# Performance work log

Hardware: AMD Instinct MI355X
Metric: run time of the kernel (lower is better)

## Reference

```python
import jax, jax.numpy as jnp
import numpy as np

B, IN_E, IN_I, D = 4096, 4096, 4096, 2048
IN_BR = 8192
BS = IN_BR // D  # block size = 4
K_E, K_I = 50, 1
E_TO_I = 50.0
BN_EPS = 1e-5


def setup_inputs() -> dict:
    key = jax.random.key(0)
    ks = jax.random.split(key, 8)
    # fan-in uniform init like nn.Linear (kaiming-uniform bound ~ 1/sqrt(in))
    def linw(k, out_f, in_f):
        b = 1.0 / np.sqrt(in_f)
        return jax.random.uniform(k, (out_f, in_f), jnp.float32, -b, b)
    return {
        "excitatory_input": jax.random.normal(ks[0], (B, IN_E), jnp.float32),
        "inhibitory_input": jax.random.normal(ks[1], (B, IN_I), jnp.float32),
        "dendrite_branch_outputs": jax.random.uniform(ks[2], (B, IN_BR), jnp.float32),
        "w_exc": linw(ks[3], D, IN_E),
        "w_inh": linw(ks[4], D, IN_I),
        "w_block": linw(ks[5], D, IN_BR),
        "bn_gamma": jnp.ones((D,), jnp.float32),
        "bn_beta": jnp.zeros((D,), jnp.float32),
    }


def _topk_linear(x, w, k):
    # keep the k largest weights per output row, zero the rest, then matmul
    idx = jax.lax.top_k(w, k)[1]                          # [D, k]
    mask = jnp.zeros_like(w).at[jnp.arange(w.shape[0])[:, None], idx].set(1.0)
    return x @ (w * mask).T                               # [B, D]


def _block_linear(x, w):
    # block-diagonal mask: row c uses columns [c*BS, (c+1)*BS)
    out_f = w.shape[0]
    wb = w.reshape(out_f, out_f, BS)[jnp.arange(out_f), jnp.arange(out_f)]  # [D, BS]
    xb = x.reshape(x.shape[0], out_f, BS)                                   # [B, D, BS]
    return jnp.einsum('bds,ds->bd', xb, wb)


def reference(excitatory_input, inhibitory_input, dendrite_branch_outputs,
              w_exc, w_inh, w_block, bn_gamma, bn_beta):
    dendrite_excitation = _topk_linear(excitatory_input, w_exc, K_E)
    dendrite_inhibition = _topk_linear(inhibitory_input, w_inh, K_I)
    dendrite_depolarization = _block_linear(dendrite_branch_outputs, w_block)
    total_excitatory = dendrite_excitation + dendrite_depolarization
    # neuron_type == 'excitatory'
    act = total_excitatory - E_TO_I * dendrite_inhibition
    # BatchNorm1d, training mode: batch stats, biased variance
    mean = jnp.mean(act, axis=0)
    var = jnp.var(act, axis=0)
    act = (act - mean) * jax.lax.rsqrt(var + BN_EPS) * bn_gamma + bn_beta
    return jax.nn.sigmoid(act)
```

## Files before the change

kernel.cpp:

```cpp
#include <hip/hip_runtime.h>
#include <hip/hip_fp16.h>

#define B_     4096
#define INE_   4096
#define INBR_  8192
#define D_     2048
#define KE_    50
#define KPAD_  52
#define CAP_   512

__device__ __forceinline__ unsigned packh2(float a, float b) {
  __half2 h = __floats2half2_rn(a, b);
  return __builtin_bit_cast(unsigned, h);
}
__device__ __forceinline__ float2 unpackh2(unsigned u) {
  __half2 h = __builtin_bit_cast(__half2, u);
  return __half22float2(h);
}

__global__ __launch_bounds__(256) void extract_diag(
    const float* __restrict__ wblock, float* __restrict__ wdiag)
{
  int d = blockIdx.x * 256 + threadIdx.x;
  float4 w = *reinterpret_cast<const float4*>(wblock + (size_t)d * (INBR_ + 4));
  reinterpret_cast<float4*>(wdiag)[d] = w;
}

__global__ __launch_bounds__(256) void topk_kernel(
    const float* __restrict__ W, int k, int kpad, float hi, float t0,
    float vscale, unsigned* __restrict__ out_off, float* __restrict__ out_val)
{
  const int row = blockIdx.x;
  const int t   = threadIdx.x;
  const float* wr = W + (size_t)row * INE_;

  __shared__ float cval[CAP_];
  __shared__ int   ccol[CAP_];
  __shared__ int   scnt;
  __shared__ int   red[4];

  float thr = t0;
  int M = 0;
  for (int attempt = 0; attempt < 8; ++attempt) {
    int local = 0;
    #pragma unroll
    for (int j = 0; j < 4; ++j) {
      float4 w4 = *reinterpret_cast<const float4*>(wr + 4 * (t + 256 * j));
      local += (w4.x > thr) + (w4.y > thr) + (w4.z > thr) + (w4.w > thr);
    }
    #pragma unroll
    for (int off = 32; off > 0; off >>= 1) local += __shfl_down(local, off);
    if ((t & 63) == 0) red[t >> 6] = local;
    __syncthreads();
    M = red[0] + red[1] + red[2] + red[3];
    __syncthreads();
    if (M >= k && M <= CAP_) break;
    if (M < k) thr = hi - (hi - thr) * 4.0f;
    else       thr = hi - (hi - thr) * 0.5f;
  }

  if (t == 0) scnt = 0;
  __syncthreads();
  #pragma unroll
  for (int j = 0; j < 4; ++j) {
    int cbase = 4 * (t + 256 * j);
    float4 w4 = *reinterpret_cast<const float4*>(wr + cbase);
    float wv[4] = {w4.x, w4.y, w4.z, w4.w};
    #pragma unroll
    for (int q = 0; q < 4; ++q) {
      if (wv[q] > thr) {
        int p = atomicAdd(&scnt, 1);
        if (p < CAP_) { cval[p] = wv[q]; ccol[p] = cbase + q; }
      }
    }
  }
  __syncthreads();
  M = scnt < CAP_ ? scnt : CAP_;

  for (int i = t; i < M; i += 256) {
    float wi = cval[i]; int ci = ccol[i];
    int rank = 0;
    for (int m = 0; m < M; ++m) {
      float wm = cval[m]; int cm = ccol[m];
      rank += (wm > wi || (wm == wi && cm < ci)) ? 1 : 0;
    }
    if (rank < k) {
      unsigned c = (unsigned)ci;
      unsigned off = ((c >> 2) << 4) | ((c & 3u) << 14);
      float    val = wi * vscale;
      if (kpad == 1) {
        out_off[row] = off;
        out_val[row] = val;
      } else {
        size_t idx = ((size_t)(rank >> 2) * D_ + row) * 4 + (rank & 3);
        out_off[idx] = off;
        out_val[idx] = val;
      }
    }
  }
  if (kpad > 1 && t < kpad - k) {
    int slot = k + t;
    size_t idx = ((size_t)(slot >> 2) * D_ + row) * 4 + (slot & 3);
    out_off[idx] = 0u;
    out_val[idx] = 0.0f;
  }
}

__device__ __forceinline__ void stage_rows(const float* __restrict__ src,
                                           unsigned* xs, int b0, int p, int Q) {
  const float* r0p = src + (size_t)(b0 + 2 * p)     * INE_;
  const float* r1p = src + (size_t)(b0 + 2 * p + 1) * INE_;
  #pragma unroll
  for (int m = 0; m < 8; ++m) {
    int c0 = 4 * Q + 512 * m;
    float4 fa = *reinterpret_cast<const float4*>(r0p + c0);
    float4 fb = *reinterpret_cast<const float4*>(r1p + c0);
    int wb = 4 * (Q + 128 * m) + p;
    xs[wb]          = packh2(fa.x, fb.x);
    xs[wb + 4096]   = packh2(fa.y, fb.y);
    xs[wb + 8192]   = packh2(fa.z, fb.z);
    xs[wb + 12288]  = packh2(fa.w, fb.w);
  }
}

#define GATH(R, OFF, WV) do {                                              \
    uint4 xq = *reinterpret_cast<const uint4*>(ldsb + (OFF));              \
    float2 f0 = unpackh2(xq.x), f1 = unpackh2(xq.y);                       \
    float2 f2 = unpackh2(xq.z), f3 = unpackh2(xq.w);                       \
    acc[R][0] = fmaf(f0.x, (WV), acc[R][0]);                               \
    acc[R][1] = fmaf(f0.y, (WV), acc[R][1]);                               \
    acc[R][2] = fmaf(f1.x, (WV), acc[R][2]);                               \
    acc[R][3] = fmaf(f1.y, (WV), acc[R][3]);                               \
    acc[R][4] = fmaf(f2.x, (WV), acc[R][4]);                               \
    acc[R][5] = fmaf(f2.y, (WV), acc[R][5]);                               \
    acc[R][6] = fmaf(f3.x, (WV), acc[R][6]);                               \
    acc[R][7] = fmaf(f3.y, (WV), acc[R][7]);                               \
  } while (0)

__global__ __launch_bounds__(512, 4) void fused_main(
    const float* __restrict__ xe, const float* __restrict__ xi,
    const float* __restrict__ xbr, const float* __restrict__ wdiag,
    const unsigned* __restrict__ soT, const float* __restrict__ veT,
    const unsigned* __restrict__ so_inh, const float* __restrict__ vi_inh,
    float* __restrict__ act)
{
  __shared__ unsigned xs[16384];
  const int t  = threadIdx.x;
  const int b0 = blockIdx.x * 8;
  const int p  = t & 3;
  const int Q  = t >> 2;

  float acc[4][8];
  #pragma unroll
  for (int r = 0; r < 4; ++r)
    #pragma unroll
    for (int b = 0; b < 8; ++b) acc[r][b] = 0.0f;

  const char* ldsb = reinterpret_cast<const char*>(xs);
  const uint4*  soT4 = reinterpret_cast<const uint4*>(soT);
  const float4* veT4 = reinterpret_cast<const float4*>(veT);

  stage_rows(xe, xs, b0, p, Q);
  __syncthreads();
  for (int ii = 0; ii < KPAD_ / 4; ++ii) {
    uint4 o[4]; float4 v[4];
    #pragma unroll
    for (int r = 0; r < 4; ++r) {
      const int d = t + 512 * r;
      o[r] = soT4[ii * D_ + d];
      v[r] = veT4[ii * D_ + d];
    }
    #pragma unroll
    for (int r = 0; r < 4; ++r) {
      GATH(r, o[r].x, v[r].x);
      GATH(r, o[r].y, v[r].y);
      GATH(r, o[r].z, v[r].z);
      GATH(r, o[r].w, v[r].w);
    }
  }
  __syncthreads();

  stage_rows(xi, xs, b0, p, Q);
  unsigned oi[4]; float vi[4];
  #pragma unroll
  for (int r = 0; r < 4; ++r) {
    const int d = t + 512 * r;
    oi[r] = so_inh[d];
    vi[r] = vi_inh[d];
  }
  __syncthreads();
  #pragma unroll
  for (int r = 0; r < 4; ++r) GATH(r, oi[r], vi[r]);

  #pragma unroll
  for (int r = 0; r < 4; ++r) {
    const int d = t + 512 * r;
    float4 wb4 = reinterpret_cast<const float4*>(wdiag)[d];
    #pragma unroll
    for (int b = 0; b < 8; ++b) {
      float4 xb4 = *reinterpret_cast<const float4*>(
          xbr + (size_t)(b0 + b) * INBR_ + 4 * d);
      acc[r][b] += xb4.x * wb4.x + xb4.y * wb4.y + xb4.z * wb4.z + xb4.w * wb4.w;
    }
  }

  #pragma unroll
  for (int r = 0; r < 4; ++r) {
    const int d = t + 512 * r;
    #pragma unroll
    for (int b = 0; b < 8; ++b)
      act[(size_t)(b0 + b) * D_ + d] = acc[r][b];
  }
}

__global__ __launch_bounds__(256) void reduce_stats(
    const float* __restrict__ act, float* __restrict__ sums,
    float* __restrict__ sumsq)
{
  const int dg = blockIdx.x & 63;
  const int rg = blockIdx.x >> 6;
  const int tx = threadIdx.x & 31;
  const int ty = threadIdx.x >> 5;
  const int d  = dg * 32 + tx;

  float s = 0.0f, s2 = 0.0f;
  #pragma unroll 4
  for (int i = 0; i < 64; ++i) {
    int row = rg * 512 + ty + 8 * i;
    float a = act[(size_t)row * D_ + d];
    s += a;
    s2 = fmaf(a, a, s2);
  }
  __shared__ float ls[2][8][32];
  ls[0][ty][tx] = s;
  ls[1][ty][tx] = s2;
  __syncthreads();
  if (ty == 0) {
    #pragma unroll
    for (int j = 1; j < 8; ++j) { s += ls[0][j][tx]; s2 += ls[1][j][tx]; }
    atomicAdd(&sums[d], s);
    atomicAdd(&sumsq[d], s2);
  }
}

__global__ __launch_bounds__(256) void finalize_stats(
    const float* __restrict__ sums, const float* __restrict__ sumsq,
    const float* __restrict__ gamma, const float* __restrict__ beta,
    float* __restrict__ scsh)
{
  int d = blockIdx.x * 256 + threadIdx.x;
  if (d < D_) {
    float mean = sums[d]  * (1.0f / B_);
    float var  = sumsq[d] * (1.0f / B_) - mean * mean;
    float rstd = rsqrtf(var + 1e-5f);
    float sc   = gamma[d] * rstd;
    scsh[2 * d]     = sc;
    scsh[2 * d + 1] = fmaf(-mean, sc, beta[d]);
  }
}

__global__ __launch_bounds__(256) void norm_sigmoid(
    float* __restrict__ act, const float* __restrict__ scsh)
{
  const int total4 = (B_ * D_) / 4;
  for (int i = blockIdx.x * blockDim.x + threadIdx.x; i < total4;
       i += gridDim.x * blockDim.x) {
    float4 a = reinterpret_cast<float4*>(act)[i];
    int d0 = (i * 4) & (D_ - 1);
    const float4* sp = reinterpret_cast<const float4*>(scsh + 2 * d0);
    float4 s0 = sp[0];
    float4 s1 = sp[1];
    float z0 = fmaf(a.x, s0.x, s0.y);
    float z1 = fmaf(a.y, s0.z, s0.w);
    float z2 = fmaf(a.z, s1.x, s1.y);
    float z3 = fmaf(a.w, s1.z, s1.w);
    a.x = 1.0f / (1.0f + __expf(-z0));
    a.y = 1.0f / (1.0f + __expf(-z1));
    a.z = 1.0f / (1.0f + __expf(-z2));
    a.w = 1.0f / (1.0f + __expf(-z3));
    reinterpret_cast<float4*>(act)[i] = a;
  }
}

extern "C" void kernel_launch(void* const* d_in, const int* in_sizes, int n_in,
                              void* d_out, int out_size, void* d_ws, size_t ws_size,
                              hipStream_t stream) {
  const float* xe    = (const float*)d_in[0];
  const float* xi    = (const float*)d_in[1];
  const float* xbr   = (const float*)d_in[2];
  const float* wexc  = (const float*)d_in[3];
  const float* winh  = (const float*)d_in[4];
  const float* wblk  = (const float*)d_in[5];
  const float* gamma = (const float*)d_in[6];
  const float* beta  = (const float*)d_in[7];
  float* act = (float*)d_out;

  char* ws = (char*)d_ws;
  unsigned* soT    = (unsigned*)(ws + 0);
  float*    veT    = (float*)   (ws + 425984);
  unsigned* so_inh = (unsigned*)(ws + 851968);
  float*    vi_inh = (float*)   (ws + 860160);
  float*    wdiag  = (float*)   (ws + 868352);
  float*    sums   = (float*)   (ws + 901120);
  float*    sumsq  = (float*)   (ws + 909312);
  float*    scsh   = (float*)   (ws + 917504);

  hipMemsetAsync(sums, 0, 2 * D_ * sizeof(float), stream);

  const float hi = 0.015625f;
  extract_diag<<<dim3(8), dim3(256), 0, stream>>>(wblk, wdiag);
  topk_kernel<<<dim3(D_), dim3(256), 0, stream>>>(
      wexc, KE_, KPAD_, hi, hi * (1.0f - 200.0f / 4096.0f), 1.0f, soT, veT);
  topk_kernel<<<dim3(D_), dim3(256), 0, stream>>>(
      winh, 1, 1, hi, hi * (1.0f - 48.0f / 4096.0f), -50.0f, so_inh, vi_inh);
  fused_main<<<dim3(B_ / 8), dim3(512), 0, stream>>>(
      xe, xi, xbr, wdiag, soT, veT, so_inh, vi_inh, act);
  reduce_stats<<<dim3(512), dim3(256), 0, stream>>>(act, sums, sumsq);
  finalize_stats<<<dim3((D_ + 255) / 256), dim3(256), 0, stream>>>(
      sums, sumsq, gamma, beta, scsh);
  norm_sigmoid<<<dim3(2048), dim3(256), 0, stream>>>(act, scsh);
}
```

Measured before the change: 140.0 us.

## Halve batch rows per block in fused gather kernel to raise occupancy

Each fused_main block now processes 4 batch rows instead of 8, which halves the LDS staging buffer (32KB instead of 64KB) and the accumulator registers. The gather offsets encoded by the top-k kernel are rescaled to the new half2-pair layout, and the launch bound requests 8 blocks per SM. This aims to raise occupancy and latency hiding for the LDS gather, but the grid doubles, so the sparse weight indices and values are loaded from global memory twice as often and each LDS load carries half as much data.

```diff
diff --git a/kernel.cpp b/kernel.cpp
--- a/kernel.cpp
+++ b/kernel.cpp
@@ -86,7 +86,7 @@
     }
     if (rank < k) {
       unsigned c = (unsigned)ci;
-      unsigned off = ((c >> 2) << 4) | ((c & 3u) << 14);
+      unsigned off = ((c >> 2) << 3) | ((c & 3u) << 13);
       float    val = wi * vscale;
       if (kpad == 1) {
         out_off[row] = off;
@@ -106,81 +106,78 @@
   }
 }
 
-__device__ __forceinline__ void stage_rows(const float* __restrict__ src,
-                                           unsigned* xs, int b0, int p, int Q) {
+__device__ __forceinline__ void stage_rows4(const float* __restrict__ src,
+                                            unsigned* xs, int b0, int p, int Q) {
   const float* r0p = src + (size_t)(b0 + 2 * p)     * INE_;
   const float* r1p = src + (size_t)(b0 + 2 * p + 1) * INE_;
   #pragma unroll
-  for (int m = 0; m < 8; ++m) {
-    int c0 = 4 * Q + 512 * m;
+  for (int m = 0; m < 4; ++m) {
+    int c0 = 4 * Q + 1024 * m;
     float4 fa = *reinterpret_cast<const float4*>(r0p + c0);
     float4 fb = *reinterpret_cast<const float4*>(r1p + c0);
-    int wb = 4 * (Q + 128 * m) + p;
-    xs[wb]          = packh2(fa.x, fb.x);
-    xs[wb + 4096]   = packh2(fa.y, fb.y);
-    xs[wb + 8192]   = packh2(fa.z, fb.z);
-    xs[wb + 12288]  = packh2(fa.w, fb.w);
-  }
-}
-
-#define GATH(R, OFF, WV) do {                                              \
-    uint4 xq = *reinterpret_cast<const uint4*>(ldsb + (OFF));              \
+    int wb = 2 * (Q + 256 * m) + p;
+    xs[wb]        = packh2(fa.x, fb.x);
+    xs[wb + 2048] = packh2(fa.y, fb.y);
+    xs[wb + 4096] = packh2(fa.z, fb.z);
+    xs[wb + 6144] = packh2(fa.w, fb.w);
+  }
+}
+
+#define GATH2(R, OFF, WV) do {                                             \
+    uint2 xq = *reinterpret_cast<const uint2*>(ldsb + (OFF));              \
     float2 f0 = unpackh2(xq.x), f1 = unpackh2(xq.y);                       \
-    float2 f2 = unpackh2(xq.z), f3 = unpackh2(xq.w);                       \
     acc[R][0] = fmaf(f0.x, (WV), acc[R][0]);                               \
     acc[R][1] = fmaf(f0.y, (WV), acc[R][1]);                               \
     acc[R][2] = fmaf(f1.x, (WV), acc[R][2]);                               \
     acc[R][3] = fmaf(f1.y, (WV), acc[R][3]);                               \
-    acc[R][4] = fmaf(f2.x, (WV), acc[R][4]);                               \
-    acc[R][5] = fmaf(f2.y, (WV), acc[R][5]);                               \
-    acc[R][6] = fmaf(f3.x, (WV), acc[R][6]);                               \
-    acc[R][7] = fmaf(f3.y, (WV), acc[R][7]);                               \
   } while (0)
 
-__global__ __launch_bounds__(512, 4) void fused_main(
+__global__ __launch_bounds__(512, 8) void fused_main(
     const float* __restrict__ xe, const float* __restrict__ xi,
     const float* __restrict__ xbr, const float* __restrict__ wdiag,
     const unsigned* __restrict__ soT, const float* __restrict__ veT,
     const unsigned* __restrict__ so_inh, const float* __restrict__ vi_inh,
     float* __restrict__ act)
 {
-  __shared__ unsigned xs[16384];
+  __shared__ unsigned xs[8192];
   const int t  = threadIdx.x;
-  const int b0 = blockIdx.x * 8;
-  const int p  = t & 3;
-  const int Q  = t >> 2;
-
-  float acc[4][8];
+  const int b0 = blockIdx.x * 4;
+  const int p  = t & 1;
+  const int Q  = t >> 1;
+
+  float acc[4][4];
   #pragma unroll
   for (int r = 0; r < 4; ++r)
     #pragma unroll
-    for (int b = 0; b < 8; ++b) acc[r][b] = 0.0f;
+    for (int b = 0; b < 4; ++b) acc[r][b] = 0.0f;
 
   const char* ldsb = reinterpret_cast<const char*>(xs);
   const uint4*  soT4 = reinterpret_cast<const uint4*>(soT);
   const float4* veT4 = reinterpret_cast<const float4*>(veT);
 
-  stage_rows(xe, xs, b0, p, Q);
+  stage_rows4(xe, xs, b0, p, Q);
   __syncthreads();
   for (int ii = 0; ii < KPAD_ / 4; ++ii) {
-    uint4 o[4]; float4 v[4];
-    #pragma unroll
-    for (int r = 0; r < 4; ++r) {
-      const int d = t + 512 * r;
-      o[r] = soT4[ii * D_ + d];
-      v[r] = veT4[ii * D_ + d];
-    }
-    #pragma unroll
-    for (int r = 0; r < 4; ++r) {
-      GATH(r, o[r].x, v[r].x);
-      GATH(r, o[r].y, v[r].y);
-      GATH(r, o[r].z, v[r].z);
-      GATH(r, o[r].w, v[r].w);
-    }
-  }
-  __syncthreads();
-
-  stage_rows(xi, xs, b0, p, Q);
+    #pragma unroll
+    for (int h = 0; h < 2; ++h) {
+      const int d0 = t + 1024 * h;
+      uint4  oa = soT4[ii * D_ + d0];
+      float4 va = veT4[ii * D_ + d0];
+      uint4  ob = soT4[ii * D_ + d0 + 512];
+      float4 vb = veT4[ii * D_ + d0 + 512];
+      GATH2(2 * h, oa.x, va.x);
+      GATH2(2 * h, oa.y, va.y);
+      GATH2(2 * h, oa.z, va.z);
+      GATH2(2 * h, oa.w, va.w);
+      GATH2(2 * h + 1, ob.x, vb.x);
+      GATH2(2 * h + 1, ob.y, vb.y);
+      GATH2(2 * h + 1, ob.z, vb.z);
+      GATH2(2 * h + 1, ob.w, vb.w);
+    }
+  }
+  __syncthreads();
+
+  stage_rows4(xi, xs, b0, p, Q);
   unsigned oi[4]; float vi[4];
   #pragma unroll
   for (int r = 0; r < 4; ++r) {
@@ -190,14 +187,14 @@
   }
   __syncthreads();
   #pragma unroll
-  for (int r = 0; r < 4; ++r) GATH(r, oi[r], vi[r]);
+  for (int r = 0; r < 4; ++r) GATH2(r, oi[r], vi[r]);
 
   #pragma unroll
   for (int r = 0; r < 4; ++r) {
     const int d = t + 512 * r;
     float4 wb4 = reinterpret_cast<const float4*>(wdiag)[d];
     #pragma unroll
-    for (int b = 0; b < 8; ++b) {
+    for (int b = 0; b < 4; ++b) {
       float4 xb4 = *reinterpret_cast<const float4*>(
           xbr + (size_t)(b0 + b) * INBR_ + 4 * d);
       acc[r][b] += xb4.x * wb4.x + xb4.y * wb4.y + xb4.z * wb4.z + xb4.w * wb4.w;
@@ -208,7 +205,7 @@
   for (int r = 0; r < 4; ++r) {
     const int d = t + 512 * r;
     #pragma unroll
-    for (int b = 0; b < 8; ++b)
+    for (int b = 0; b < 4; ++b)
       act[(size_t)(b0 + b) * D_ + d] = acc[r][b];
   }
 }
@@ -313,7 +310,7 @@
       wexc, KE_, KPAD_, hi, hi * (1.0f - 200.0f / 4096.0f), 1.0f, soT, veT);
   topk_kernel<<<dim3(D_), dim3(256), 0, stream>>>(
       winh, 1, 1, hi, hi * (1.0f - 48.0f / 4096.0f), -50.0f, so_inh, vi_inh);
-  fused_main<<<dim3(B_ / 8), dim3(512), 0, stream>>>(
+  fused_main<<<dim3(B_ / 4), dim3(512), 0, stream>>>(
       xe, xi, xbr, wdiag, soT, veT, so_inh, vi_inh, act);
   reduce_stats<<<dim3(512), dim3(256), 0, stream>>>(act, sums, sumsq);
   finalize_stats<<<dim3((D_ + 255) / 256), dim3(256), 0, stream>>>(
```

New measurement: 143.2 us. 2.2% more time.
